# Kernel tuning notes

Measured on AMD Instinct MI355X. Metric: run time of the kernel, lower is better.

Reference implementation:

```python
import jax, jax.numpy as jnp
import numpy as np

NH = 4  # num_heads

def _layernorm(x, w, eps=1e-5):
    mu = x.mean(-1, keepdims=True)
    var = x.var(-1, keepdims=True)
    return (x - mu) * jax.lax.rsqrt(var + eps) * w

def _mh_layernorm(y, w, eps=1e-5):
    # per-head layernorm over head_dim; y: (B,S,nh,hd), w: (nh,hd)
    mu = y.mean(-1, keepdims=True)
    var = y.var(-1, keepdims=True)
    return (y - mu) * jax.lax.rsqrt(var + eps) * w

def _slstm_layer(h, conv_w, conv_b, Wgates, R, Rb):
    B, S, D = h.shape
    nh = NH; hd = D // nh; K = conv_w.shape[1]
    # causal depthwise conv1d + SiLU (i/f gate preprocessing)
    lhs = jnp.transpose(h, (0, 2, 1))              # (B, D, S)
    rhs = conv_w[:, None, :]                       # (D, 1, K)
    xc = jax.lax.conv_general_dilated(
        lhs, rhs, window_strides=(1,), padding=[(K - 1, 0)],
        feature_group_count=D,
        dimension_numbers=("NCH", "OIH", "NCH")) + conv_b[None, :, None]
    xc = jax.nn.silu(jnp.transpose(xc, (0, 2, 1)))  # (B, S, D)

    hh = h.reshape(B, S, nh, hd)
    cc = xc.reshape(B, S, nh, hd)
    # headwise (block-diagonal) gate projections: i,f from conv branch; z,o from x
    wi = jnp.einsum('bsnd,nde->bsne', cc, Wgates[0])
    wf = jnp.einsum('bsnd,nde->bsne', cc, Wgates[1])
    wz = jnp.einsum('bsnd,nde->bsne', hh, Wgates[2])
    wo = jnp.einsum('bsnd,nde->bsne', hh, Wgates[3])
    Wx = jnp.stack([wi, wf, wz, wo], axis=2)       # (B,S,4,nh,hd)
    Wx = jnp.moveaxis(Wx, 1, 0)                    # (S,B,4,nh,hd)

    def step(carry, inp):
        hprev, c, n, m = carry                     # each (B,nh,hd)
        wx, t = inp
        r = jnp.einsum('bnd,ndge->bgne', hprev, R)  # headwise recurrent: (B,4,nh,hd)
        raw = wx + r + Rb[None]                    # (B,4,nh,hd)
        ir, fr, zr, orr = raw[:, 0], raw[:, 1], raw[:, 2], raw[:, 3]
        # exponential gating with running-max stabilizer (vanilla sLSTM backend)
        logfplusm = m + jax.nn.log_sigmoid(fr)
        mnew = jnp.where(t == 0, ir, jnp.maximum(ir, logfplusm))
        ig = jnp.exp(ir - mnew)
        fg = jnp.exp(logfplusm - mnew)
        cnew = fg * c + ig * jnp.tanh(zr)
        nnew = fg * n + ig
        hnew = jax.nn.sigmoid(orr) * cnew / nnew
        return (hnew, cnew, nnew, mnew), hnew

    z0 = jnp.zeros((B, nh, hd), h.dtype)
    _, ys = jax.lax.scan(step, (z0, z0, z0, z0), (Wx, jnp.arange(S)))
    return jnp.moveaxis(ys, 0, 1)                  # (B,S,nh,hd)

def _forward(x, E, ln1_w, conv_w, conv_b, Wgates, R, Rb, gn_w, ln2_w,
             ffn_up, ffn_down, post_w, fc_w, fc_b):
    B, S = x.shape
    D = E.shape[1]; nh = NH; hd = D // nh
    h = E[x]                                        # (B,S,D) embedding
    # sLSTM block: pre-norm -> sLSTM layer -> multi-head groupnorm -> residual
    y = _slstm_layer(_layernorm(h, ln1_w), conv_w, conv_b, Wgates, R, Rb)
    y = _mh_layernorm(y, gn_w.reshape(nh, hd)).reshape(B, S, D)
    h = h + y
    # gated feedforward (proj_factor 1.3, gelu), pre-norm + residual
    u = _layernorm(h, ln2_w) @ ffn_up               # (B,S,2*1344)
    gate, upv = jnp.split(u, 2, axis=-1)
    h = h + (jax.nn.gelu(gate, approximate=False) * upv) @ ffn_down
    # post-stack layernorm, last token, classifier head
    h = _layernorm(h, post_w)
    return jax.nn.sigmoid(h[:, -1, :] @ fc_w + fc_b)  # (B,1)

def setup_inputs() -> dict:
    key = jax.random.key(0)
    ks = jax.random.split(key, 10)
    V, D, B, S = 32000, 1024, 32, 512
    nh, hd, K, up = NH, 1024 // NH, 4, 1344
    s = lambda k, shape, sc: jax.random.normal(k, shape, jnp.float32) * sc
    E = s(ks[0], (V, D), 1.0).at[0].set(0.0)  # padding_idx=0 zeroed
    return {
        "x": jax.random.randint(ks[1], (B, S), 0, V),
        "E": E,
        "ln1_w": jnp.ones((D,), jnp.float32),
        "conv_w": s(ks[2], (D, K), 0.3),
        "conv_b": jnp.zeros((D,), jnp.float32),
        "Wgates": s(ks[3], (4, nh, hd, hd), 1.0 / np.sqrt(hd)),
        "R": s(ks[4], (nh, hd, 4, hd), 1.0 / np.sqrt(hd)),
        "Rb": s(ks[5], (4, nh, hd), 0.1),
        "gn_w": jnp.ones((D,), jnp.float32),
        "ln2_w": jnp.ones((D,), jnp.float32),
        "ffn_up": s(ks[6], (D, 2 * up), 1.0 / np.sqrt(D)),
        "ffn_down": s(ks[7], (up, D), 1.0 / np.sqrt(up)),
        "post_w": jnp.ones((D,), jnp.float32),
        "fc_w": s(ks[8], (D, 1), 1.0 / np.sqrt(D)),
        "fc_b": jnp.zeros((1,), jnp.float32),
    }

def reference(x, E, ln1_w, conv_w, conv_b, Wgates, R, Rb, gn_w, ln2_w,
              ffn_up, ffn_down, post_w, fc_w, fc_b):
    return _forward(x, E, ln1_w, conv_w, conv_b, Wgates, R, Rb, gn_w, ln2_w,
                    ffn_up, ffn_down, post_w, fc_w, fc_b)
```

## Files before the change

kernel.cpp:

```cpp
#include <hip/hip_runtime.h>
#include <math.h>

typedef unsigned short u16;

constexpr size_t OFF_HLN   = 0;
constexpr size_t OFF_CC    = 33554432;
constexpr size_t OFF_WXB   = 67108864;
constexpr size_t OFF_RT    = 201326592;
constexpr size_t OFF_WHP   = 203423744;
constexpr size_t OFF_HLAST = 205520896;
constexpr size_t OFF_YLAST = 205651968;
constexpr size_t OFF_POOL  = 205783040;

constexpr int P_LN1  = 0;
constexpr int P_CW   = 1024;
constexpr int P_CB   = 5120;
constexpr int P_WG   = 6144;
constexpr int P_R    = 1054720;
constexpr int P_RB   = 2103296;
constexpr int P_GN   = 2107392;
constexpr int P_LN2  = 2108416;
constexpr int P_UP   = 2109440;
constexpr int P_DN   = 4861952;
constexpr int P_POST = 6238208;
constexpr int P_FC   = 6239232;
constexpr int P_FCB  = 6240256;

__device__ __forceinline__ float bf(u16 u) {
    return __uint_as_float(((unsigned)u) << 16);
}
__device__ __forceinline__ u16 f2bf(float x) {
    unsigned u = __float_as_uint(x);
    unsigned r = (u + 0x7fffu + ((u >> 16) & 1u)) >> 16;
    return (u16)r;
}
__device__ __forceinline__ float h16f(u16 u) {
    return (float)__builtin_bit_cast(_Float16, u);
}
__device__ __forceinline__ u16 f2h(float x) {
    return __builtin_bit_cast(u16, (_Float16)x);
}
__device__ __forceinline__ bool is_fp32_mode(const unsigned* probe) {
    return probe[0] == 0x3F800000u;
}

typedef _Float16 h2_t __attribute__((ext_vector_type(2)));

__device__ __forceinline__ float dot2f(unsigned a, unsigned b, float c) {
#if __has_builtin(__builtin_amdgcn_fdot2)
    return __builtin_amdgcn_fdot2(__builtin_bit_cast(h2_t, a),
                                  __builtin_bit_cast(h2_t, b), c, false);
#else
    h2_t av = __builtin_bit_cast(h2_t, a);
    h2_t bv = __builtin_bit_cast(h2_t, b);
    c += (float)av.x * (float)bv.x;
    c += (float)av.y * (float)bv.y;
    return c;
#endif
}

__device__ __forceinline__ unsigned pk2h(float lo, float hi) {
    unsigned short a = __builtin_bit_cast(unsigned short, (_Float16)lo);
    unsigned short b = __builtin_bit_cast(unsigned short, (_Float16)hi);
    return (((unsigned)b) << 16) | (unsigned)a;
}

__device__ __forceinline__ float2 block_sum2(float a, float b) {
    __shared__ float ra[4], rb[4];
    for (int o = 32; o > 0; o >>= 1) {
        a += __shfl_down(a, o);
        b += __shfl_down(b, o);
    }
    int w = threadIdx.x >> 6;
    if ((threadIdx.x & 63) == 0) { ra[w] = a; rb[w] = b; }
    __syncthreads();
    float sa = ra[0] + ra[1] + ra[2] + ra[3];
    float sb = rb[0] + rb[1] + rb[2] + rb[3];
    __syncthreads();
    return make_float2(sa, sb);
}

__global__ __launch_bounds__(256) void cvt_weights(
        const void* p0, const void* p1, const void* p2, const void* p3,
        const void* p4, const void* p5, const void* p6, const void* p7,
        const void* p8, const void* p9, const void* p10, const void* p11,
        const void* p12, float* pool) {
    bool fp32 = is_fp32_mode((const unsigned*)p0);
    const void* ps[13] = {p0, p1, p2, p3, p4, p5, p6, p7, p8, p9, p10, p11, p12};
    const int ns[13] = {1024, 4096, 1024, 1048576, 1048576, 4096, 1024,
                        1024, 2752512, 1376256, 1024, 1024, 1};
    const int po[13] = {P_LN1, P_CW, P_CB, P_WG, P_R, P_RB, P_GN,
                        P_LN2, P_UP, P_DN, P_POST, P_FC, P_FCB};
    int gid = blockIdx.x * 256 + threadIdx.x;
    int stride = gridDim.x * 256;
    #pragma unroll 1
    for (int w = 0; w < 13; ++w) {
        float* dst = pool + po[w];
        int n = ns[w];
        if (fp32) {
            const float* src = (const float*)ps[w];
            for (int i = gid; i < n; i += stride) dst[i] = src[i];
        } else {
            const u16* src = (const u16*)ps[w];
            for (int i = gid; i < n; i += stride) dst[i] = bf(src[i]);
        }
    }
}

__global__ __launch_bounds__(256) void transpose_R(const float* __restrict__ Rsrc,
                                                   unsigned* __restrict__ Rt) {
    int gid = blockIdx.x * 256 + threadIdx.x;
    int e = gid & 255;
    int k = (gid >> 8) & 127;
    int n = gid >> 15;
    size_t base0 = ((size_t)(n * 256 + 2 * k) * 4) << 8;
    size_t base1 = ((size_t)(n * 256 + 2 * k + 1) * 4) << 8;
    uint4 q;
    q.x = pk2h(Rsrc[base0 + (0 << 8) + e], Rsrc[base1 + (0 << 8) + e]);
    q.y = pk2h(Rsrc[base0 + (1 << 8) + e], Rsrc[base1 + (1 << 8) + e]);
    q.z = pk2h(Rsrc[base0 + (2 << 8) + e], Rsrc[base1 + (2 << 8) + e]);
    q.w = pk2h(Rsrc[base0 + (3 << 8) + e], Rsrc[base1 + (3 << 8) + e]);
    ((uint4*)Rt)[gid] = q;
}

__global__ __launch_bounds__(256) void pack_W(const float* __restrict__ Wsrc,
                                              unsigned* __restrict__ Whp) {
    int o = blockIdx.x * 256 + threadIdx.x;
    int e = o & 255;
    int kp = (o >> 8) & 127;
    int gn = o >> 15;
    const float* src = Wsrc + ((size_t)(gn * 256 + 2 * kp) << 8) + e;
    Whp[o] = pk2h(src[0], src[256]);
}

__global__ __launch_bounds__(256) void embed_ln1(const int* __restrict__ x,
                                                 const void* E,
                                                 const float* __restrict__ pool,
                                                 const unsigned* __restrict__ probe,
                                                 u16* __restrict__ hln,
                                                 float* __restrict__ hlast) {
    bool fp32 = is_fp32_mode(probe);
    int row = blockIdx.x;
    int t = threadIdx.x;
    int idx = x[row];
    float v0, v1, v2, v3;
    if (fp32) {
        const float* e = ((const float*)E) + (size_t)idx * 1024;
        v0 = e[t]; v1 = e[t + 256]; v2 = e[t + 512]; v3 = e[t + 768];
    } else {
        const u16* e = ((const u16*)E) + (size_t)idx * 1024;
        v0 = bf(e[t]); v1 = bf(e[t + 256]); v2 = bf(e[t + 512]); v3 = bf(e[t + 768]);
    }
    float2 s = block_sum2(v0 + v1 + v2 + v3, v0 * v0 + v1 * v1 + v2 * v2 + v3 * v3);
    float mu = s.x * (1.f / 1024.f);
    float rs = rsqrtf(s.y * (1.f / 1024.f) - mu * mu + 1e-5f);
    const float* w = pool + P_LN1;
    u16* o = hln + (size_t)row * 1024;
    o[t]       = f2h((v0 - mu) * rs * w[t]);
    o[t + 256] = f2h((v1 - mu) * rs * w[t + 256]);
    o[t + 512] = f2h((v2 - mu) * rs * w[t + 512]);
    o[t + 768] = f2h((v3 - mu) * rs * w[t + 768]);
    if ((row & 511) == 511) {
        float* hl = hlast + (size_t)(row >> 9) * 1024;
        hl[t] = v0; hl[t + 256] = v1; hl[t + 512] = v2; hl[t + 768] = v3;
    }
}

__global__ __launch_bounds__(256) void conv_silu(const u16* __restrict__ hln,
                                                 const float* __restrict__ pool,
                                                 u16* __restrict__ cc) {
    int gid = blockIdx.x * 256 + threadIdx.x;
    int d = gid & 1023;
    int s = (gid >> 10) & 511;
    const float* cw = pool + P_CW;
    float acc = pool[P_CB + d];
    #pragma unroll
    for (int k = 0; k < 4; ++k) {
        int sp = s - 3 + k;
        if (sp >= 0) acc += h16f(hln[gid - (size_t)(3 - k) * 1024]) * cw[d * 4 + k];
    }
    float sg = 1.f / (1.f + expf(-acc));
    cc[gid] = f2h(acc * sg);
}

__global__ __launch_bounds__(256) void wx_gemm(const u16* __restrict__ cc,
                                               const u16* __restrict__ hln,
                                               const unsigned* __restrict__ Whp,
                                               u16* __restrict__ Wxb) {
    __shared__ unsigned Alds[16][72];
    __shared__ unsigned Wlds[16][256];
    int rt = blockIdx.x;
    int n = blockIdx.y;
    int g = blockIdx.z;
    const u16* A = (g < 2) ? cc : hln;
    int tid = threadIdx.x;
    int cl = tid & 31;
    int rg = tid >> 5;
    float acc[8][8] = {};
    int r0 = rt * 64;
    const unsigned* Wg = Whp + ((size_t)(g * 4 + n) << 15);
    int ai = tid >> 2;
    int aj = (tid & 3) * 4;

    for (int k0 = 0; k0 < 128; k0 += 16) {
        {
            const unsigned* asrc =
                (const unsigned*)(A + (size_t)(r0 + ai) * 1024 + n * 256) + k0 + aj;
            uint4 av = *(const uint4*)asrc;
            Alds[aj + 0][ai] = av.x; Alds[aj + 1][ai] = av.y;
            Alds[aj + 2][ai] = av.z; Alds[aj + 3][ai] = av.w;
        }
        {
            const uint4* wsrc = (const uint4*)(Wg + (size_t)k0 * 256);
            uint4* wdst = (uint4*)&Wlds[0][0];
            #pragma unroll
            for (int q = 0; q < 4; ++q) wdst[q * 256 + tid] = wsrc[q * 256 + tid];
        }
        __syncthreads();
        #pragma unroll 8
        for (int kp = 0; kp < 16; ++kp) {
            uint4 aa = *(const uint4*)&Alds[kp][rg * 8];
            uint4 ab = *(const uint4*)&Alds[kp][rg * 8 + 4];
            unsigned a_[8] = {aa.x, aa.y, aa.z, aa.w, ab.x, ab.y, ab.z, ab.w};
            unsigned w_[8];
            #pragma unroll
            for (int j = 0; j < 8; ++j) w_[j] = Wlds[kp][cl + 32 * j];
            #pragma unroll
            for (int i = 0; i < 8; ++i)
                #pragma unroll
                for (int j = 0; j < 8; ++j) acc[i][j] = dot2f(a_[i], w_[j], acc[i][j]);
        }
        __syncthreads();
    }
    #pragma unroll
    for (int i = 0; i < 8; ++i) {
        int r = r0 + rg * 8 + i;
        int bb = r >> 9;
        int s = r & 511;
        size_t base = ((size_t)((s * 32 + bb) * 4 + n) << 10) + (g << 8);
        #pragma unroll
        for (int j = 0; j < 8; ++j) {
            Wxb[base + cl + 32 * j] = f2bf(acc[i][j]);
        }
    }
}

#define ACC4(hb, RV)                          \
    {                                         \
        r0 = dot2f((hb), (RV).x, r0);         \
        r1 = dot2f((hb), (RV).y, r1);         \
        r2 = dot2f((hb), (RV).z, r2);         \
        r3 = dot2f((hb), (RV).w, r3);         \
    }

__global__ __attribute__((amdgpu_flat_work_group_size(512, 512),
                          amdgpu_waves_per_eu(1, 2)))
void scan_kernel(const u16* __restrict__ Wxb,
                 const unsigned* __restrict__ Rt,
                 const float* __restrict__ pool,
                 float* __restrict__ ylast) {
    int b = blockIdx.x >> 2;
    int n = blockIdx.x & 3;
    int t = threadIdx.x;
    int p = t >> 8;
    int e = t & 255;

    __shared__ __align__(16) unsigned hp[128];
    __shared__ uint4 Rl4[16][512];
    __shared__ float rb4s[4][256];
    __shared__ float ra[4], rq[4];

    const uint4* Rt4 = (const uint4*)Rt;
    int kbase = (n << 7) + (p << 6);

    uint4 Rr[48];
    #pragma unroll
    for (int kk = 0; kk < 48; ++kk)
        Rr[kk] = Rt4[((kbase + kk) << 8) | e];
    #pragma unroll
    for (int kk = 0; kk < 16; ++kk)
        Rl4[kk][t] = Rt4[((kbase + 48 + kk) << 8) | e];

    const uint4* hp4 = (const uint4*)hp;
    int p16 = p << 4;

    float rb0 = 0.f, rb1 = 0.f, rb2 = 0.f, rb3 = 0.f;
    if (p == 0) {
        rb0 = pool[P_RB + 0 * 1024 + (n << 8) + e];
        rb1 = pool[P_RB + 1 * 1024 + (n << 8) + e];
        rb2 = pool[P_RB + 2 * 1024 + (n << 8) + e];
        rb3 = pool[P_RB + 3 * 1024 + (n << 8) + e];
    }
    if (t < 128) hp[t] = 0u;
    float c = 0.f, nrm = 1.f, m = 0.f, h = 0.f;
    __syncthreads();

    #pragma unroll 1
    for (int s = 0; s < 512; ++s) {
        u16 w0 = 0, w1 = 0, w2 = 0, w3 = 0;
        if (p == 0) {
            const u16* wxp = Wxb + (((size_t)(s * 32 + b) * 4 + n) << 10) + e;
            w0 = wxp[0]; w1 = wxp[256]; w2 = wxp[512]; w3 = wxp[768];
        }
        float r0 = 0.f, r1 = 0.f, r2 = 0.f, r3 = 0.f;
        #pragma unroll
        for (int q = 0; q < 12; ++q) {
            uint4 hv = hp4[p16 + q];
            ACC4(hv.x, Rr[4 * q + 0]); ACC4(hv.y, Rr[4 * q + 1]);
            ACC4(hv.z, Rr[4 * q + 2]); ACC4(hv.w, Rr[4 * q + 3]);
        }
        #pragma unroll
        for (int q = 0; q < 4; ++q) {
            uint4 hv = hp4[p16 + 12 + q];
            uint4 q0 = Rl4[4 * q + 0][t], q1 = Rl4[4 * q + 1][t];
            uint4 q2 = Rl4[4 * q + 2][t], q3 = Rl4[4 * q + 3][t];
            ACC4(hv.x, q0); ACC4(hv.y, q1); ACC4(hv.z, q2); ACC4(hv.w, q3);
        }
        if (p != 0) {
            rb4s[0][e] = r0; rb4s[1][e] = r1; rb4s[2][e] = r2; rb4s[3][e] = r3;
        }
        __syncthreads();
        if (p == 0) {
            float ir  = bf(w0) + r0 + rb4s[0][e] + rb0;
            float fr  = bf(w1) + r1 + rb4s[1][e] + rb1;
            float zr  = bf(w2) + r2 + rb4s[2][e] + rb2;
            float orr = bf(w3) + r3 + rb4s[3][e] + rb3;
            float qf = __expf(-fabsf(fr));
            float ls = fminf(fr, 0.f) - __logf(1.f + qf);
            float lfm = m + ls;
            float mnew = (s == 0) ? ir : fmaxf(ir, lfm);
            float ig = __expf(ir - mnew);
            float fg = __expf(lfm - mnew);
            float qz = __expf(-2.f * fabsf(zr));
            float tz = (1.f - qz) / (1.f + qz);
            tz = (zr < 0.f) ? -tz : tz;
            c   = (s == 0) ? (ig * tz) : (fg * c + ig * tz);
            nrm = (s == 0) ? ig : (fg * nrm + ig);
            m = mnew;
            float og = 1.f / (1.f + __expf(-orr));
            h = og * c / nrm;
            ((_Float16*)hp)[e] = (_Float16)h;
        }
        __syncthreads();
    }

    if (p == 0) {
        float a = h, q = h * h;
        for (int o = 32; o > 0; o >>= 1) {
            a += __shfl_down(a, o);
            q += __shfl_down(q, o);
        }
        if ((t & 63) == 0) { ra[t >> 6] = a; rq[t >> 6] = q; }
    }
    __syncthreads();
    if (p == 0) {
        float sa = ra[0] + ra[1] + ra[2] + ra[3];
        float sq = rq[0] + rq[1] + rq[2] + rq[3];
        float mu = sa * (1.f / 256.f);
        float rs = rsqrtf(sq * (1.f / 256.f) - mu * mu + 1e-5f);
        ylast[((size_t)(b * 4 + n) << 8) + e] = (h - mu) * rs * pool[P_GN + (n << 8) + e];
    }
}

__global__ __launch_bounds__(256) void tail_kernel(const float* __restrict__ hlast,
                                                   const float* __restrict__ ylast,
                                                   const float* __restrict__ pool,
                                                   const unsigned* __restrict__ probe,
                                                   void* out) {
    int b = blockIdx.x;
    int t = threadIdx.x;
    __shared__ float hf[1024];
    __shared__ float hn[1024];
    __shared__ float u[2688];
    __shared__ float vv[1344];
    for (int i = t; i < 1024; i += 256)
        hf[i] = hlast[(size_t)b * 1024 + i] + ylast[(size_t)b * 1024 + i];
    __syncthreads();
    float sa = 0.f, sb = 0.f;
    for (int i = t; i < 1024; i += 256) { float xv = hf[i]; sa += xv; sb += xv * xv; }
    float2 s = block_sum2(sa, sb);
    float mu = s.x * (1.f / 1024.f);
    float rs = rsqrtf(s.y * (1.f / 1024.f) - mu * mu + 1e-5f);
    for (int i = t; i < 1024; i += 256) hn[i] = (hf[i] - mu) * rs * pool[P_LN2 + i];
    __syncthreads();
    const float* upw = pool + P_UP;
    for (int j = t; j < 2688; j += 256) {
        float a = 0.f;
        for (int d = 0; d < 1024; d += 4) {
            a += hn[d]     * upw[(size_t)d * 2688 + j];
            a += hn[d + 1] * upw[(size_t)(d + 1) * 2688 + j];
            a += hn[d + 2] * upw[(size_t)(d + 2) * 2688 + j];
            a += hn[d + 3] * upw[(size_t)(d + 3) * 2688 + j];
        }
        u[j] = a;
    }
    __syncthreads();
    for (int j = t; j < 1344; j += 256) {
        float g = u[j];
        float ge = 0.5f * g * (1.f + erff(g * 0.70710678118654752f));
        vv[j] = ge * u[1344 + j];
    }
    __syncthreads();
    const float* dnw = pool + P_DN;
    for (int dcol = t; dcol < 1024; dcol += 256) {
        float a = 0.f;
        for (int j = 0; j < 1344; j += 4) {
            a += vv[j]     * dnw[(size_t)j * 1024 + dcol];
            a += vv[j + 1] * dnw[(size_t)(j + 1) * 1024 + dcol];
            a += vv[j + 2] * dnw[(size_t)(j + 2) * 1024 + dcol];
            a += vv[j + 3] * dnw[(size_t)(j + 3) * 1024 + dcol];
        }
        hn[dcol] = hf[dcol] + a;
    }
    __syncthreads();
    sa = 0.f; sb = 0.f;
    for (int i = t; i < 1024; i += 256) { float xv = hn[i]; sa += xv; sb += xv * xv; }
    s = block_sum2(sa, sb);
    mu = s.x * (1.f / 1024.f);
    rs = rsqrtf(s.y * (1.f / 1024.f) - mu * mu + 1e-5f);
    float part = 0.f;
    for (int i = t; i < 1024; i += 256)
        part += (hn[i] - mu) * rs * pool[P_POST + i] * pool[P_FC + i];
    float2 tot = block_sum2(part, 0.f);
    if (t == 0) {
        float logit = tot.x + pool[P_FCB];
        float sig = 1.f / (1.f + expf(-logit));
        if (is_fp32_mode(probe)) ((float*)out)[b] = sig;
        else                     ((u16*)out)[b] = f2bf(sig);
    }
}

extern "C" void kernel_launch(void* const* d_in, const int* in_sizes, int n_in,
                              void* d_out, int out_size, void* d_ws, size_t ws_size,
                              hipStream_t stream) {
    const int* x = (const int*)d_in[0];
    const void* E = d_in[1];
    const unsigned* probe = (const unsigned*)d_in[2];

    char* ws = (char*)d_ws;
    u16*      hln   = (u16*)(ws + OFF_HLN);
    u16*      cc    = (u16*)(ws + OFF_CC);
    u16*      Wxb   = (u16*)(ws + OFF_WXB);
    unsigned* Rt    = (unsigned*)(ws + OFF_RT);
    unsigned* Whp   = (unsigned*)(ws + OFF_WHP);
    float*    hlast = (float*)(ws + OFF_HLAST);
    float*    ylast = (float*)(ws + OFF_YLAST);
    float*    pool  = (float*)(ws + OFF_POOL);

    hipLaunchKernelGGL(cvt_weights, dim3(512), dim3(256), 0, stream,
                       d_in[2], d_in[3], d_in[4], d_in[5], d_in[6], d_in[7], d_in[8],
                       d_in[9], d_in[10], d_in[11], d_in[12], d_in[13], d_in[14], pool);
    hipLaunchKernelGGL(transpose_R, dim3(512), dim3(256), 0, stream, pool + P_R, Rt);
    hipLaunchKernelGGL(pack_W, dim3(2048), dim3(256), 0, stream, pool + P_WG, Whp);
    hipLaunchKernelGGL(embed_ln1, dim3(16384), dim3(256), 0, stream,
                       x, E, pool, probe, hln, hlast);
    hipLaunchKernelGGL(conv_silu, dim3(65536), dim3(256), 0, stream, hln, pool, cc);
    hipLaunchKernelGGL(wx_gemm, dim3(256, 4, 4), dim3(256), 0, stream, cc, hln, Whp, Wxb);
    hipLaunchKernelGGL(scan_kernel, dim3(128), dim3(512), 0, stream, Wxb, Rt, pool, ylast);
    hipLaunchKernelGGL(tail_kernel, dim3(32), dim3(256), 0, stream,
                       hlast, ylast, pool, probe, d_out);
}
```

Measured before the change: 1.999 ms.

## Run sLSTM scan with one thread per output and double-buffered hidden state

The recurrent scan kernel drops from 512 threads (two K-halves combined through shared memory) to 256 threads that each compute the full 128-step dot product. It keeps 112 R rows in registers and 16 in LDS, and double-buffers the fp16 hidden state so each time step needs one barrier instead of two. This removes the partial-sum exchange and one barrier per step on a latency-bound serial loop. In exchange each thread does twice the dot-product work and needs many more registers (448 VGPRs for R alone), which risks spills.

```diff
diff --git a/kernel.cpp b/kernel.cpp
--- a/kernel.cpp
+++ b/kernel.cpp
@@ -253,113 +253,85 @@
         r3 = dot2f((hb), (RV).w, r3);         \
     }
 
-__global__ __attribute__((amdgpu_flat_work_group_size(512, 512),
-                          amdgpu_waves_per_eu(1, 2)))
+__global__ __attribute__((amdgpu_flat_work_group_size(256, 256),
+                          amdgpu_waves_per_eu(1, 1)))
 void scan_kernel(const u16* __restrict__ Wxb,
                  const unsigned* __restrict__ Rt,
                  const float* __restrict__ pool,
                  float* __restrict__ ylast) {
     int b = blockIdx.x >> 2;
     int n = blockIdx.x & 3;
-    int t = threadIdx.x;
-    int p = t >> 8;
-    int e = t & 255;
-
-    __shared__ __align__(16) unsigned hp[128];
-    __shared__ uint4 Rl4[16][512];
-    __shared__ float rb4s[4][256];
-    __shared__ float ra[4], rq[4];
+    int e = threadIdx.x;
+
+    __shared__ __align__(16) unsigned hp2[2][128];
+    __shared__ uint4 Rl4[16][256];
 
     const uint4* Rt4 = (const uint4*)Rt;
-    int kbase = (n << 7) + (p << 6);
-
-    uint4 Rr[48];
+    int kbase = n << 7;
+
+    uint4 Rr[112];
     #pragma unroll
-    for (int kk = 0; kk < 48; ++kk)
+    for (int kk = 0; kk < 112; ++kk)
         Rr[kk] = Rt4[((kbase + kk) << 8) | e];
     #pragma unroll
     for (int kk = 0; kk < 16; ++kk)
-        Rl4[kk][t] = Rt4[((kbase + 48 + kk) << 8) | e];
-
-    const uint4* hp4 = (const uint4*)hp;
-    int p16 = p << 4;
-
-    float rb0 = 0.f, rb1 = 0.f, rb2 = 0.f, rb3 = 0.f;
-    if (p == 0) {
-        rb0 = pool[P_RB + 0 * 1024 + (n << 8) + e];
-        rb1 = pool[P_RB + 1 * 1024 + (n << 8) + e];
-        rb2 = pool[P_RB + 2 * 1024 + (n << 8) + e];
-        rb3 = pool[P_RB + 3 * 1024 + (n << 8) + e];
-    }
-    if (t < 128) hp[t] = 0u;
+        Rl4[kk][e] = Rt4[((kbase + 112 + kk) << 8) | e];
+
+    float rb0 = pool[P_RB + 0 * 1024 + (n << 8) + e];
+    float rb1 = pool[P_RB + 1 * 1024 + (n << 8) + e];
+    float rb2 = pool[P_RB + 2 * 1024 + (n << 8) + e];
+    float rb3 = pool[P_RB + 3 * 1024 + (n << 8) + e];
+
+    if (e < 128) hp2[0][e] = 0u;
     float c = 0.f, nrm = 1.f, m = 0.f, h = 0.f;
     __syncthreads();
 
     #pragma unroll 1
     for (int s = 0; s < 512; ++s) {
-        u16 w0 = 0, w1 = 0, w2 = 0, w3 = 0;
-        if (p == 0) {
-            const u16* wxp = Wxb + (((size_t)(s * 32 + b) * 4 + n) << 10) + e;
-            w0 = wxp[0]; w1 = wxp[256]; w2 = wxp[512]; w3 = wxp[768];
-        }
+        const u16* wxp = Wxb + (((size_t)(s * 32 + b) * 4 + n) << 10) + e;
+        u16 w0 = wxp[0], w1 = wxp[256], w2 = wxp[512], w3 = wxp[768];
+
+        const uint4* hcur = (const uint4*)hp2[s & 1];
         float r0 = 0.f, r1 = 0.f, r2 = 0.f, r3 = 0.f;
         #pragma unroll
-        for (int q = 0; q < 12; ++q) {
-            uint4 hv = hp4[p16 + q];
+        for (int q = 0; q < 28; ++q) {
+            uint4 hv = hcur[q];
             ACC4(hv.x, Rr[4 * q + 0]); ACC4(hv.y, Rr[4 * q + 1]);
             ACC4(hv.z, Rr[4 * q + 2]); ACC4(hv.w, Rr[4 * q + 3]);
         }
         #pragma unroll
         for (int q = 0; q < 4; ++q) {
-            uint4 hv = hp4[p16 + 12 + q];
-            uint4 q0 = Rl4[4 * q + 0][t], q1 = Rl4[4 * q + 1][t];
-            uint4 q2 = Rl4[4 * q + 2][t], q3 = Rl4[4 * q + 3][t];
+            uint4 hv = hcur[28 + q];
+            uint4 q0 = Rl4[4 * q + 0][e], q1 = Rl4[4 * q + 1][e];
+            uint4 q2 = Rl4[4 * q + 2][e], q3 = Rl4[4 * q + 3][e];
             ACC4(hv.x, q0); ACC4(hv.y, q1); ACC4(hv.z, q2); ACC4(hv.w, q3);
         }
-        if (p != 0) {
-            rb4s[0][e] = r0; rb4s[1][e] = r1; rb4s[2][e] = r2; rb4s[3][e] = r3;
-        }
+        float ir  = bf(w0) + r0 + rb0;
+        float fr  = bf(w1) + r1 + rb1;
+        float zr  = bf(w2) + r2 + rb2;
+        float orr = bf(w3) + r3 + rb3;
+        float qf = __expf(-fabsf(fr));
+        float ls = fminf(fr, 0.f) - __logf(1.f + qf);
+        float lfm = m + ls;
+        float mnew = (s == 0) ? ir : fmaxf(ir, lfm);
+        float ig = __expf(ir - mnew);
+        float fg = __expf(lfm - mnew);
+        float qz = __expf(-2.f * fabsf(zr));
+        float tz = (1.f - qz) / (1.f + qz);
+        tz = (zr < 0.f) ? -tz : tz;
+        c   = (s == 0) ? (ig * tz) : (fg * c + ig * tz);
+        nrm = (s == 0) ? ig : (fg * nrm + ig);
+        m = mnew;
+        float og = 1.f / (1.f + __expf(-orr));
+        h = og * c / nrm;
+        ((_Float16*)hp2[(s + 1) & 1])[e] = (_Float16)h;
         __syncthreads();
-        if (p == 0) {
-            float ir  = bf(w0) + r0 + rb4s[0][e] + rb0;
-            float fr  = bf(w1) + r1 + rb4s[1][e] + rb1;
-            float zr  = bf(w2) + r2 + rb4s[2][e] + rb2;
-            float orr = bf(w3) + r3 + rb4s[3][e] + rb3;
-            float qf = __expf(-fabsf(fr));
-            float ls = fminf(fr, 0.f) - __logf(1.f + qf);
-            float lfm = m + ls;
-            float mnew = (s == 0) ? ir : fmaxf(ir, lfm);
-            float ig = __expf(ir - mnew);
-            float fg = __expf(lfm - mnew);
-            float qz = __expf(-2.f * fabsf(zr));
-            float tz = (1.f - qz) / (1.f + qz);
-            tz = (zr < 0.f) ? -tz : tz;
-            c   = (s == 0) ? (ig * tz) : (fg * c + ig * tz);
-            nrm = (s == 0) ? ig : (fg * nrm + ig);
-            m = mnew;
-            float og = 1.f / (1.f + __expf(-orr));
-            h = og * c / nrm;
-            ((_Float16*)hp)[e] = (_Float16)h;
-        }
-        __syncthreads();
-    }
-
-    if (p == 0) {
-        float a = h, q = h * h;
-        for (int o = 32; o > 0; o >>= 1) {
-            a += __shfl_down(a, o);
-            q += __shfl_down(q, o);
-        }
-        if ((t & 63) == 0) { ra[t >> 6] = a; rq[t >> 6] = q; }
-    }
-    __syncthreads();
-    if (p == 0) {
-        float sa = ra[0] + ra[1] + ra[2] + ra[3];
-        float sq = rq[0] + rq[1] + rq[2] + rq[3];
-        float mu = sa * (1.f / 256.f);
-        float rs = rsqrtf(sq * (1.f / 256.f) - mu * mu + 1e-5f);
-        ylast[((size_t)(b * 4 + n) << 8) + e] = (h - mu) * rs * pool[P_GN + (n << 8) + e];
-    }
+    }
+
+    float2 s2 = block_sum2(h, h * h);
+    float mu = s2.x * (1.f / 256.f);
+    float rs = rsqrtf(s2.y * (1.f / 256.f) - mu * mu + 1e-5f);
+    ylast[((size_t)(b * 4 + n) << 8) + e] = (h - mu) * rs * pool[P_GN + (n << 8) + e];
 }
 
 __global__ __launch_bounds__(256) void tail_kernel(const float* __restrict__ hlast,
@@ -456,7 +428,7 @@
                        x, E, pool, probe, hln, hlast);
     hipLaunchKernelGGL(conv_silu, dim3(65536), dim3(256), 0, stream, hln, pool, cc);
     hipLaunchKernelGGL(wx_gemm, dim3(256, 4, 4), dim3(256), 0, stream, cc, hln, Whp, Wxb);
-    hipLaunchKernelGGL(scan_kernel, dim3(128), dim3(512), 0, stream, Wxb, Rt, pool, ylast);
+    hipLaunchKernelGGL(scan_kernel, dim3(128), dim3(256), 0, stream, Wxb, Rt, pool, ylast);
     hipLaunchKernelGGL(tail_kernel, dim3(32), dim3(256), 0, stream,
                        hlast, ylast, pool, probe, d_out);
 }
```

Measured after the change: 3.049 ms. +52.6%, slower.

## Use MFMA for the gate projection GEMM and vectorize conv_silu

Applied to the files above, without the earlier changes.

The headwise gate projection GEMM now uses the 16x16x32 f16 MFMA instruction instead of packed dot2 FMAs. The whole 64x256 A tile is staged in LDS once, and B fragments are read directly from a newly transposed f16 weight layout produced by pack_Wt. The causal conv+SiLU kernel now handles 8 channels per thread with 128-bit loads and stores and uses fast exp. The aim is to cut the compute cost of the Wx precompute; it adds a larger LDS footprint and uncached global reads of the weights per wave.

```diff
diff --git a/kernel.cpp b/kernel.cpp
--- a/kernel.cpp
+++ b/kernel.cpp
@@ -7,7 +7,7 @@
 constexpr size_t OFF_CC    = 33554432;
 constexpr size_t OFF_WXB   = 67108864;
 constexpr size_t OFF_RT    = 201326592;
-constexpr size_t OFF_WHP   = 203423744;
+constexpr size_t OFF_WT    = 203423744;
 constexpr size_t OFF_HLAST = 205520896;
 constexpr size_t OFF_YLAST = 205651968;
 constexpr size_t OFF_POOL  = 205783040;
@@ -45,6 +45,8 @@
 }
 
 typedef _Float16 h2_t __attribute__((ext_vector_type(2)));
+typedef _Float16 v8h __attribute__((ext_vector_type(8)));
+typedef float v4f __attribute__((ext_vector_type(4)));
 
 __device__ __forceinline__ float dot2f(unsigned a, unsigned b, float c) {
 #if __has_builtin(__builtin_amdgcn_fdot2)
@@ -123,14 +125,13 @@
     ((uint4*)Rt)[gid] = q;
 }
 
-__global__ __launch_bounds__(256) void pack_W(const float* __restrict__ Wsrc,
-                                              unsigned* __restrict__ Whp) {
+__global__ __launch_bounds__(256) void pack_Wt(const float* __restrict__ Wsrc,
+                                               u16* __restrict__ Wt) {
     int o = blockIdx.x * 256 + threadIdx.x;
-    int e = o & 255;
-    int kp = (o >> 8) & 127;
-    int gn = o >> 15;
-    const float* src = Wsrc + ((size_t)(gn * 256 + 2 * kp) << 8) + e;
-    Whp[o] = pk2h(src[0], src[256]);
+    int k = o & 255;
+    int e = (o >> 8) & 255;
+    int gn = o >> 16;
+    Wt[o] = f2h(Wsrc[((((size_t)gn << 8) | k) << 8) | e]);
 }
 
 __global__ __launch_bounds__(256) void embed_ln1(const int* __restrict__ x,
@@ -170,77 +171,83 @@
                                                  const float* __restrict__ pool,
                                                  u16* __restrict__ cc) {
     int gid = blockIdx.x * 256 + threadIdx.x;
-    int d = gid & 1023;
-    int s = (gid >> 10) & 511;
-    const float* cw = pool + P_CW;
-    float acc = pool[P_CB + d];
+    int d8 = gid & 127;
+    int sb = gid >> 7;
+    int s = sb & 511;
+    size_t base = ((size_t)sb << 10) + ((size_t)d8 << 3);
+    uint4 z = make_uint4(0, 0, 0, 0);
+    uint4 v0 = *(const uint4*)&hln[base];
+    uint4 v1 = (s >= 1) ? *(const uint4*)&hln[base - 1024] : z;
+    uint4 v2 = (s >= 2) ? *(const uint4*)&hln[base - 2048] : z;
+    uint4 v3 = (s >= 3) ? *(const uint4*)&hln[base - 3072] : z;
+    const u16* p0 = (const u16*)&v0; const u16* p1 = (const u16*)&v1;
+    const u16* p2 = (const u16*)&v2; const u16* p3 = (const u16*)&v3;
+    int d0 = d8 << 3;
+    u16 out[8];
     #pragma unroll
-    for (int k = 0; k < 4; ++k) {
-        int sp = s - 3 + k;
-        if (sp >= 0) acc += h16f(hln[gid - (size_t)(3 - k) * 1024]) * cw[d * 4 + k];
-    }
-    float sg = 1.f / (1.f + expf(-acc));
-    cc[gid] = f2h(acc * sg);
+    for (int j = 0; j < 8; ++j) {
+        int d = d0 + j;
+        float4 cw = *(const float4*)&pool[P_CW + d * 4];
+        float acc = pool[P_CB + d]
+                  + h16f(p3[j]) * cw.x + h16f(p2[j]) * cw.y
+                  + h16f(p1[j]) * cw.z + h16f(p0[j]) * cw.w;
+        float sg = 1.f / (1.f + __expf(-acc));
+        out[j] = f2h(acc * sg);
+    }
+    *(uint4*)&cc[base] = *(const uint4*)out;
 }
 
 __global__ __launch_bounds__(256) void wx_gemm(const u16* __restrict__ cc,
                                                const u16* __restrict__ hln,
-                                               const unsigned* __restrict__ Whp,
+                                               const u16* __restrict__ Wt,
                                                u16* __restrict__ Wxb) {
-    __shared__ unsigned Alds[16][72];
-    __shared__ unsigned Wlds[16][256];
-    int rt = blockIdx.x;
-    int n = blockIdx.y;
-    int g = blockIdx.z;
+    __shared__ u16 Alds[64][264];
+    int rt = blockIdx.x, gn = blockIdx.y;
+    int g = gn >> 2, n = gn & 3;
     const u16* A = (g < 2) ? cc : hln;
     int tid = threadIdx.x;
-    int cl = tid & 31;
-    int rg = tid >> 5;
-    float acc[8][8] = {};
+    int w = tid >> 6, l = tid & 63;
+    int lr = l & 15, kg = l >> 4;
     int r0 = rt * 64;
-    const unsigned* Wg = Whp + ((size_t)(g * 4 + n) << 15);
-    int ai = tid >> 2;
-    int aj = (tid & 3) * 4;
-
-    for (int k0 = 0; k0 < 128; k0 += 16) {
-        {
-            const unsigned* asrc =
-                (const unsigned*)(A + (size_t)(r0 + ai) * 1024 + n * 256) + k0 + aj;
-            uint4 av = *(const uint4*)asrc;
-            Alds[aj + 0][ai] = av.x; Alds[aj + 1][ai] = av.y;
-            Alds[aj + 2][ai] = av.z; Alds[aj + 3][ai] = av.w;
-        }
-        {
-            const uint4* wsrc = (const uint4*)(Wg + (size_t)k0 * 256);
-            uint4* wdst = (uint4*)&Wlds[0][0];
+    {
+        int row = tid >> 2;
+        int kk0 = (tid & 3) * 64;
+        const u16* src = A + (size_t)(r0 + row) * 1024 + n * 256 + kk0;
+        #pragma unroll
+        for (int q = 0; q < 8; ++q) {
+            uint4 v = ((const uint4*)src)[q];
+            *(uint4*)&Alds[row][kk0 + q * 8] = v;
+        }
+    }
+    __syncthreads();
+    const u16* Wg = Wt + ((size_t)gn << 16);
+    v4f acc[4][4] = {};
+    #pragma unroll
+    for (int k0 = 0; k0 < 256; k0 += 32) {
+        v8h af[4];
+        #pragma unroll
+        for (int r4 = 0; r4 < 4; ++r4)
+            af[r4] = *(const v8h*)&Alds[r4 * 16 + lr][k0 + (kg << 3)];
+        #pragma unroll
+        for (int et = 0; et < 4; ++et) {
+            v8h bfr = *(const v8h*)&Wg[(size_t)((w << 6) + (et << 4) + lr) * 256 + k0 + (kg << 3)];
             #pragma unroll
-            for (int q = 0; q < 4; ++q) wdst[q * 256 + tid] = wsrc[q * 256 + tid];
-        }
-        __syncthreads();
-        #pragma unroll 8
-        for (int kp = 0; kp < 16; ++kp) {
-            uint4 aa = *(const uint4*)&Alds[kp][rg * 8];
-            uint4 ab = *(const uint4*)&Alds[kp][rg * 8 + 4];
-            unsigned a_[8] = {aa.x, aa.y, aa.z, aa.w, ab.x, ab.y, ab.z, ab.w};
-            unsigned w_[8];
+            for (int r4 = 0; r4 < 4; ++r4)
+                acc[r4][et] = __builtin_amdgcn_mfma_f32_16x16x32_f16(af[r4], bfr,
+                                                                     acc[r4][et], 0, 0, 0);
+        }
+    }
+    #pragma unroll
+    for (int r4 = 0; r4 < 4; ++r4) {
+        #pragma unroll
+        for (int t = 0; t < 4; ++t) {
+            int r = r0 + r4 * 16 + (kg << 2) + t;
+            int bb = r >> 9;
+            int s = r & 511;
+            size_t base = ((size_t)((s * 32 + bb) * 4 + n) << 10) + (g << 8);
             #pragma unroll
-            for (int j = 0; j < 8; ++j) w_[j] = Wlds[kp][cl + 32 * j];
-            #pragma unroll
-            for (int i = 0; i < 8; ++i)
-                #pragma unroll
-                for (int j = 0; j < 8; ++j) acc[i][j] = dot2f(a_[i], w_[j], acc[i][j]);
-        }
-        __syncthreads();
-    }
-    #pragma unroll
-    for (int i = 0; i < 8; ++i) {
-        int r = r0 + rg * 8 + i;
-        int bb = r >> 9;
-        int s = r & 511;
-        size_t base = ((size_t)((s * 32 + bb) * 4 + n) << 10) + (g << 8);
-        #pragma unroll
-        for (int j = 0; j < 8; ++j) {
-            Wxb[base + cl + 32 * j] = f2bf(acc[i][j]);
+            for (int et = 0; et < 4; ++et)
+                Wxb[base + (w << 6) + (et << 4) + lr] = f2bf(acc[r4][et][t]);
         }
     }
 }
@@ -442,7 +449,7 @@
     u16*      cc    = (u16*)(ws + OFF_CC);
     u16*      Wxb   = (u16*)(ws + OFF_WXB);
     unsigned* Rt    = (unsigned*)(ws + OFF_RT);
-    unsigned* Whp   = (unsigned*)(ws + OFF_WHP);
+    u16*      Wt    = (u16*)(ws + OFF_WT);
     float*    hlast = (float*)(ws + OFF_HLAST);
     float*    ylast = (float*)(ws + OFF_YLAST);
     float*    pool  = (float*)(ws + OFF_POOL);
@@ -451,11 +458,11 @@
                        d_in[2], d_in[3], d_in[4], d_in[5], d_in[6], d_in[7], d_in[8],
                        d_in[9], d_in[10], d_in[11], d_in[12], d_in[13], d_in[14], pool);
     hipLaunchKernelGGL(transpose_R, dim3(512), dim3(256), 0, stream, pool + P_R, Rt);
-    hipLaunchKernelGGL(pack_W, dim3(2048), dim3(256), 0, stream, pool + P_WG, Whp);
+    hipLaunchKernelGGL(pack_Wt, dim3(4096), dim3(256), 0, stream, pool + P_WG, Wt);
     hipLaunchKernelGGL(embed_ln1, dim3(16384), dim3(256), 0, stream,
                        x, E, pool, probe, hln, hlast);
-    hipLaunchKernelGGL(conv_silu, dim3(65536), dim3(256), 0, stream, hln, pool, cc);
-    hipLaunchKernelGGL(wx_gemm, dim3(256, 4, 4), dim3(256), 0, stream, cc, hln, Whp, Wxb);
+    hipLaunchKernelGGL(conv_silu, dim3(8192), dim3(256), 0, stream, hln, pool, cc);
+    hipLaunchKernelGGL(wx_gemm, dim3(256, 16), dim3(256), 0, stream, cc, hln, Wt, Wxb);
     hipLaunchKernelGGL(scan_kernel, dim3(128), dim3(512), 0, stream, Wxb, Rt, pool, ylast);
     hipLaunchKernelGGL(tail_kernel, dim3(32), dim3(256), 0, stream,
                        hlast, ylast, pool, probe, d_out);
```

Measured after the change: 1.812 ms. 9.3% less time.
